# Kernel tuning notes

Hardware: AMD Instinct MI355X
Metric: run time of the kernel (lower is better)

Reference implementation:

```python
import jax, jax.numpy as jnp
import numpy as np

EPS = 1e-5  # torch F.layer_norm default

def setup_inputs() -> dict:
    key = jax.random.key(0)
    k_h, k_v = jax.random.split(key)
    B, S, d, rank = 4, 4096, 2048, 8
    h = jax.random.normal(k_h, (B, S, d), dtype=jnp.float32)
    gamma = jnp.ones((d,), dtype=jnp.float32)
    beta = jnp.zeros((d,), dtype=jnp.float32)
    V = jax.random.normal(k_v, (rank, d), dtype=jnp.float32) * 0.01
    eta = jnp.asarray(0.1, dtype=jnp.float32)
    return {"h": h, "gamma": gamma, "beta": beta, "V": V, "eta": eta}

def reference(h, gamma, beta, V, eta):
    # LayerNorm over last dim, no affine (torch F.layer_norm with only normalized_shape)
    mu = jnp.mean(h, axis=-1, keepdims=True)
    var = jnp.mean((h - mu) ** 2, axis=-1, keepdims=True)  # biased var, matches torch
    h_hat = (h - mu) * jax.lax.rsqrt(var + EPS)
    # low-rank diffusion: h_hat @ (V^T V) == (h_hat @ V^T) @ V, O(n*d*rank)
    proj = jnp.einsum('bsr,rd->bsd', jnp.einsum('bsd,rd->bsr', h_hat, V), V)
    delta_h = h_hat - proj
    e_curv = jnp.sum(delta_h ** 2, axis=-1)  # [B, S]
    eta_c = jnp.clip(eta, 0.0, 0.5)
    h_smooth = h_hat - eta_c * delta_h
    out = h_smooth * gamma + beta
    return out, e_curv
```

## Files before the change

### kernel.cpp

```cpp
#include <hip/hip_runtime.h>
#include <hip/hip_bf16.h>


constexpr int D       = 2048;
constexpr int RANK    = 8;
constexpr int BLOCK   = 256;
constexpr int ROWS_PB = 4;
constexpr float LN_EPS = 1e-5f;

using f2  = __attribute__((ext_vector_type(2))) float;
using f4v = __attribute__((ext_vector_type(4))) float;

__device__ __forceinline__ f2 f2fma(f2 a, f2 b, f2 c) {
    return __builtin_elementwise_fma(a, b, c);
}

__device__ __forceinline__ void nt_store4(float* p, float x, float y, float z, float w) {
    f4v v = {x, y, z, w};
    __builtin_nontemporal_store(v, reinterpret_cast<f4v*>(p));
}

__device__ __forceinline__ void barrier_lds() {
    asm volatile("s_waitcnt lgkmcnt(0)\n\ts_barrier" ::: "memory");
}

__device__ __forceinline__ float ordadd(float a, float b) {
    float r;
    asm volatile("v_add_f32 %0, %1, %2" : "=v"(r) : "v"(a), "v"(b));
    return r;
}

#define DPP_STAGE(v, N, MODS)                                                   \
    _Pragma("unroll")                                                           \
    for (int _n = 0; _n < N; ++_n)                                              \
        asm volatile("v_add_f32_dpp %0, %0, %0 " MODS : "+v"(v[_n]));

template<int N>
__device__ __forceinline__ void dpp_sum64_batch(float (&v)[N]) {
    static_assert(N >= 4, "need N>=4 for hazard distance");
    DPP_STAGE(v, N, "row_shr:1 row_mask:0xf bank_mask:0xf bound_ctrl:0")
    DPP_STAGE(v, N, "row_shr:2 row_mask:0xf bank_mask:0xf bound_ctrl:0")
    DPP_STAGE(v, N, "row_shr:4 row_mask:0xf bank_mask:0xf bound_ctrl:0")
    DPP_STAGE(v, N, "row_shr:8 row_mask:0xf bank_mask:0xf bound_ctrl:0")
    DPP_STAGE(v, N, "row_bcast:15 row_mask:0xa bank_mask:0xf bound_ctrl:0")
    DPP_STAGE(v, N, "row_bcast:31 row_mask:0xc bank_mask:0xf bound_ctrl:0")
}

template<int N>
__device__ __forceinline__ void qp_sum4_batch(float (&v)[N]) {
    static_assert(N >= 4, "need N>=4 for hazard distance");
    asm volatile("s_nop 1");
    DPP_STAGE(v, N, "quad_perm:[1,0,3,2] row_mask:0xf bank_mask:0xf bound_ctrl:0")
    DPP_STAGE(v, N, "quad_perm:[2,3,0,1] row_mask:0xf bank_mask:0xf bound_ctrl:0")
}

__global__ __launch_bounds__(BLOCK, 2)
void lbonorm_kernel(const float* __restrict__ h,
                    const float* __restrict__ gamma,
                    const float* __restrict__ beta,
                    const float* __restrict__ V,
                    const float* __restrict__ eta_p,
                    float* __restrict__ out,
                    float* __restrict__ e_out)
{
    const int t    = threadIdx.x;
    const int lane = t & 63;
    const int wave = t >> 6;

    const int c0 = t * 4;
    const int c1 = D / 2 + t * 4;

    __shared__ __align__(16) float red[ROWS_PB][4][12];
    __shared__ __align__(16) float ered[4][RANK];

    const size_t row0 = (size_t)blockIdx.x * ROWS_PB;

    f2 vreg[4][RANK];
    #pragma unroll
    for (int r = 0; r < RANK; ++r) {
        float4 a = *reinterpret_cast<const float4*>(V + (size_t)r * D + c0);
        float4 b = *reinterpret_cast<const float4*>(V + (size_t)r * D + c1);
        vreg[0][r] = f2{a.x, a.y}; vreg[1][r] = f2{a.z, a.w};
        vreg[2][r] = f2{b.x, b.y}; vreg[3][r] = f2{b.z, b.w};
    }
    const float4 g0 = *reinterpret_cast<const float4*>(gamma + c0);
    const float4 g1 = *reinterpret_cast<const float4*>(gamma + c1);
    const float4 bb0 = *reinterpret_cast<const float4*>(beta + c0);
    const float4 bb1 = *reinterpret_cast<const float4*>(beta + c1);
    const f2 gam[4] = {f2{g0.x,g0.y}, f2{g0.z,g0.w}, f2{g1.x,g1.y}, f2{g1.z,g1.w}};
    const f2 bet[4] = {f2{bb0.x,bb0.y}, f2{bb0.z,bb0.w}, f2{bb1.x,bb1.y}, f2{bb1.z,bb1.w}};
    const float eta = fminf(fmaxf(eta_p[0], 0.0f), 0.5f);

    float4 hx[ROWS_PB][2];
    #pragma unroll
    for (int r = 0; r < ROWS_PB; ++r) {
        hx[r][0] = *reinterpret_cast<const float4*>(h + (row0 + r) * (size_t)D + c0);
        hx[r][1] = *reinterpret_cast<const float4*>(h + (row0 + r) * (size_t)D + c1);
    }

    float vsum[RANK];
    {
        float vs[RANK];
        #pragma unroll
        for (int r = 0; r < RANK; ++r) {
            f2 v = (vreg[0][r] + vreg[1][r]) + (vreg[2][r] + vreg[3][r]);
            vs[r] = ordadd(v.x, v.y);
        }
        dpp_sum64_batch(vs);
        if (lane == 63) {
            float4* dst = reinterpret_cast<float4*>(&ered[wave][0]);
            dst[0] = make_float4(vs[0], vs[1], vs[2], vs[3]);
            dst[1] = make_float4(vs[4], vs[5], vs[6], vs[7]);
        }
        barrier_lds();
        const float4* src = reinterpret_cast<const float4*>(&ered[lane & 3][0]);
        const float4 qa = src[0], qb = src[1];
        float qv[8] = {qa.x, qa.y, qa.z, qa.w, qb.x, qb.y, qb.z, qb.w};
        qp_sum4_batch(qv);
        #pragma unroll
        for (int k = 0; k < RANK; ++k) vsum[k] = qv[k];
    }

    #pragma unroll
    for (int r = 0; r < ROWS_PB; ++r) {
        const f2 h2[4] = {f2{hx[r][0].x, hx[r][0].y}, f2{hx[r][0].z, hx[r][0].w},
                          f2{hx[r][1].x, hx[r][1].y}, f2{hx[r][1].z, hx[r][1].w}};
        float vals[10];
        {
            f2 s  = (h2[0] + h2[1]) + (h2[2] + h2[3]);
            f2 s2 = f2fma(h2[0], h2[0], f2fma(h2[1], h2[1],
                    f2fma(h2[2], h2[2], h2[3] * h2[3])));
            vals[0] = ordadd(s.x, s.y);
            vals[1] = ordadd(s2.x, s2.y);
            #pragma unroll
            for (int k = 0; k < RANK; ++k) {
                f2 d = f2fma(h2[0], vreg[0][k], f2fma(h2[1], vreg[1][k],
                       f2fma(h2[2], vreg[2][k], h2[3] * vreg[3][k])));
                vals[2 + k] = ordadd(d.x, d.y);
            }
        }
        dpp_sum64_batch(vals);

        if (lane == 63) {
            float4* dst = reinterpret_cast<float4*>(&red[r][wave][0]);
            dst[0] = make_float4(vals[0], vals[1], vals[2], vals[3]);
            dst[1] = make_float4(vals[4], vals[5], vals[6], vals[7]);
            dst[2] = make_float4(vals[8], vals[9], 0.f, 0.f);
        }
    }

    barrier_lds();

    float er[ROWS_PB];
    #pragma unroll
    for (int r = 0; r < ROWS_PB; ++r) {
        const float4* src = reinterpret_cast<const float4*>(&red[r][lane & 3][0]);
        const float4 q0 = src[0], q1 = src[1], q2 = src[2];
        float qv[10] = {q0.x, q0.y, q0.z, q0.w, q1.x, q1.y, q1.z, q1.w, q2.x, q2.y};
        qp_sum4_batch(qv);

        const float mu  = qv[0] * (1.0f / D);
        const float var = fmaxf(qv[1] * (1.0f / D) - mu * mu, 0.0f);
        const float inv = rsqrtf(var + LN_EPS);
        f2 c2[RANK];
        #pragma unroll
        for (int k = 0; k < RANK; ++k) {
            const float c = inv * (qv[2 + k] - mu * vsum[k]);
            c2[k] = f2{c, c};
        }

        const f2 h2[4] = {f2{hx[r][0].x, hx[r][0].y}, f2{hx[r][0].z, hx[r][0].w},
                          f2{hx[r][1].x, hx[r][1].y}, f2{hx[r][1].z, hx[r][1].w}};
        const f2 inv2  = f2{inv, inv};
        const f2 nmi2  = f2{-mu * inv, -mu * inv};
        const f2 neta2 = f2{-eta, -eta};
        f2 e2 = f2{0.f, 0.f};
        f2 ov[4];
        #pragma unroll
        for (int k = 0; k < 4; ++k) {
            const f2 hh = f2fma(h2[k], inv2, nmi2);
            f2 pr = c2[0] * vreg[k][0];
            #pragma unroll
            for (int q = 1; q < RANK; ++q) pr = f2fma(c2[q], vreg[k][q], pr);
            const f2 dl = hh - pr;
            e2 = f2fma(dl, dl, e2);
            const f2 sm = f2fma(neta2, dl, hh);
            ov[k] = f2fma(sm, gam[k], bet[k]);
        }

        float* orow = out + (row0 + r) * (size_t)D;
        nt_store4(orow + c0, ov[0].x, ov[0].y, ov[1].x, ov[1].y);
        nt_store4(orow + c1, ov[2].x, ov[2].y, ov[3].x, ov[3].y);

        er[r] = ordadd(e2.x, e2.y);
    }

    dpp_sum64_batch(er);
    if (lane == 63) {
        float4* dst = reinterpret_cast<float4*>(&ered[wave][0]);
        dst[0] = make_float4(er[0], er[1], er[2], er[3]);
    }
    barrier_lds();
    if (t < ROWS_PB) {
        const float e = (ered[0][t] + ered[1][t]) + (ered[2][t] + ered[3][t]);
        e_out[row0 + t] = e;
    }
}

extern "C" void kernel_launch(void* const* d_in, const int* in_sizes, int n_in,
                              void* d_out, int out_size, void* d_ws, size_t ws_size,
                              hipStream_t stream) {
    const float* h     = (const float*)d_in[0];
    const float* gamma = (const float*)d_in[1];
    const float* beta  = (const float*)d_in[2];
    const float* V     = (const float*)d_in[3];
    const float* eta   = (const float*)d_in[4];
    float* out = (float*)d_out;

    const int d = in_sizes[1];
    const long long rows = in_sizes[0] / d;
    float* e_out = out + (size_t)rows * d;

    dim3 grid((unsigned)(rows / ROWS_PB));
    lbonorm_kernel<<<grid, BLOCK, 0, stream>>>(h, gamma, beta, V, eta, out, e_out);
}
```

Before: 49.27 us.

## Process multiple row chunks per block with double-buffered register prefetch

```diff
diff --git a/kernel.cpp b/kernel.cpp
--- a/kernel.cpp
+++ b/kernel.cpp
@@ -5,7 +5,8 @@
 constexpr int D       = 2048;
 constexpr int RANK    = 8;
 constexpr int BLOCK   = 256;
-constexpr int ROWS_PB = 4;
+constexpr int ROWS_PC = 4;
+constexpr int NCHUNK  = 8;
 constexpr float LN_EPS = 1e-5f;
 
 using f2  = __attribute__((ext_vector_type(2))) float;
@@ -70,10 +71,10 @@
     const int c0 = t * 4;
     const int c1 = D / 2 + t * 4;
 
-    __shared__ __align__(16) float red[ROWS_PB][4][12];
-    __shared__ __align__(16) float ered[4][RANK];
-
-    const size_t row0 = (size_t)blockIdx.x * ROWS_PB;
+    __shared__ __align__(16) float red[2][ROWS_PC][4][12];
+    __shared__ __align__(16) float ered[4][ROWS_PC * NCHUNK];
+
+    const size_t row0 = (size_t)blockIdx.x * (ROWS_PC * NCHUNK);
 
     f2 vreg[4][RANK];
     #pragma unroll
@@ -91,11 +92,11 @@
     const f2 bet[4] = {f2{bb0.x,bb0.y}, f2{bb0.z,bb0.w}, f2{bb1.x,bb1.y}, f2{bb1.z,bb1.w}};
     const float eta = fminf(fmaxf(eta_p[0], 0.0f), 0.5f);
 
-    float4 hx[ROWS_PB][2];
+    float4 hxA[ROWS_PC][2], hxB[ROWS_PC][2];
     #pragma unroll
-    for (int r = 0; r < ROWS_PB; ++r) {
-        hx[r][0] = *reinterpret_cast<const float4*>(h + (row0 + r) * (size_t)D + c0);
-        hx[r][1] = *reinterpret_cast<const float4*>(h + (row0 + r) * (size_t)D + c1);
+    for (int r = 0; r < ROWS_PC; ++r) {
+        hxA[r][0] = *reinterpret_cast<const float4*>(h + (row0 + r) * (size_t)D + c0);
+        hxA[r][1] = *reinterpret_cast<const float4*>(h + (row0 + r) * (size_t)D + c1);
     }
 
     float vsum[RANK];
@@ -122,86 +123,101 @@
     }
 
     #pragma unroll
-    for (int r = 0; r < ROWS_PB; ++r) {
-        const f2 h2[4] = {f2{hx[r][0].x, hx[r][0].y}, f2{hx[r][0].z, hx[r][0].w},
-                          f2{hx[r][1].x, hx[r][1].y}, f2{hx[r][1].z, hx[r][1].w}};
-        float vals[10];
-        {
-            f2 s  = (h2[0] + h2[1]) + (h2[2] + h2[3]);
-            f2 s2 = f2fma(h2[0], h2[0], f2fma(h2[1], h2[1],
-                    f2fma(h2[2], h2[2], h2[3] * h2[3])));
-            vals[0] = ordadd(s.x, s.y);
-            vals[1] = ordadd(s2.x, s2.y);
+    for (int c = 0; c < NCHUNK; ++c) {
+        float4 (&cur)[ROWS_PC][2] = (c & 1) ? hxB : hxA;
+        float4 (&nxt)[ROWS_PC][2] = (c & 1) ? hxA : hxB;
+
+        if (c + 1 < NCHUNK) {
+            const size_t nrow = row0 + (size_t)(c + 1) * ROWS_PC;
+            #pragma unroll
+            for (int r = 0; r < ROWS_PC; ++r) {
+                nxt[r][0] = *reinterpret_cast<const float4*>(h + (nrow + r) * (size_t)D + c0);
+                nxt[r][1] = *reinterpret_cast<const float4*>(h + (nrow + r) * (size_t)D + c1);
+            }
+        }
+
+        #pragma unroll
+        for (int r = 0; r < ROWS_PC; ++r) {
+            const f2 h2[4] = {f2{cur[r][0].x, cur[r][0].y}, f2{cur[r][0].z, cur[r][0].w},
+                              f2{cur[r][1].x, cur[r][1].y}, f2{cur[r][1].z, cur[r][1].w}};
+            float vals[10];
+            {
+                f2 s  = (h2[0] + h2[1]) + (h2[2] + h2[3]);
+                f2 s2 = f2fma(h2[0], h2[0], f2fma(h2[1], h2[1],
+                        f2fma(h2[2], h2[2], h2[3] * h2[3])));
+                vals[0] = ordadd(s.x, s.y);
+                vals[1] = ordadd(s2.x, s2.y);
+                #pragma unroll
+                for (int k = 0; k < RANK; ++k) {
+                    f2 d = f2fma(h2[0], vreg[0][k], f2fma(h2[1], vreg[1][k],
+                           f2fma(h2[2], vreg[2][k], h2[3] * vreg[3][k])));
+                    vals[2 + k] = ordadd(d.x, d.y);
+                }
+            }
+            dpp_sum64_batch(vals);
+
+            if (lane == 63) {
+                float4* dst = reinterpret_cast<float4*>(&red[c & 1][r][wave][0]);
+                dst[0] = make_float4(vals[0], vals[1], vals[2], vals[3]);
+                dst[1] = make_float4(vals[4], vals[5], vals[6], vals[7]);
+                dst[2] = make_float4(vals[8], vals[9], 0.f, 0.f);
+            }
+        }
+
+        barrier_lds();
+
+        float er[ROWS_PC];
+        #pragma unroll
+        for (int r = 0; r < ROWS_PC; ++r) {
+            const float4* src = reinterpret_cast<const float4*>(&red[c & 1][r][lane & 3][0]);
+            const float4 q0 = src[0], q1 = src[1], q2 = src[2];
+            float qv[10] = {q0.x, q0.y, q0.z, q0.w, q1.x, q1.y, q1.z, q1.w, q2.x, q2.y};
+            qp_sum4_batch(qv);
+
+            const float mu  = qv[0] * (1.0f / D);
+            const float var = fmaxf(qv[1] * (1.0f / D) - mu * mu, 0.0f);
+            const float inv = rsqrtf(var + LN_EPS);
+            f2 c2[RANK];
             #pragma unroll
             for (int k = 0; k < RANK; ++k) {
-                f2 d = f2fma(h2[0], vreg[0][k], f2fma(h2[1], vreg[1][k],
-                       f2fma(h2[2], vreg[2][k], h2[3] * vreg[3][k])));
-                vals[2 + k] = ordadd(d.x, d.y);
-            }
-        }
-        dpp_sum64_batch(vals);
-
-        if (lane == 63) {
-            float4* dst = reinterpret_cast<float4*>(&red[r][wave][0]);
-            dst[0] = make_float4(vals[0], vals[1], vals[2], vals[3]);
-            dst[1] = make_float4(vals[4], vals[5], vals[6], vals[7]);
-            dst[2] = make_float4(vals[8], vals[9], 0.f, 0.f);
-        }
+                const float cc = inv * (qv[2 + k] - mu * vsum[k]);
+                c2[k] = f2{cc, cc};
+            }
+
+            const f2 h2[4] = {f2{cur[r][0].x, cur[r][0].y}, f2{cur[r][0].z, cur[r][0].w},
+                              f2{cur[r][1].x, cur[r][1].y}, f2{cur[r][1].z, cur[r][1].w}};
+            const f2 inv2  = f2{inv, inv};
+            const f2 nmi2  = f2{-mu * inv, -mu * inv};
+            const f2 neta2 = f2{-eta, -eta};
+            f2 e2 = f2{0.f, 0.f};
+            f2 ov[4];
+            #pragma unroll
+            for (int k = 0; k < 4; ++k) {
+                const f2 hh = f2fma(h2[k], inv2, nmi2);
+                f2 pr = c2[0] * vreg[k][0];
+                #pragma unroll
+                for (int q = 1; q < RANK; ++q) pr = f2fma(c2[q], vreg[k][q], pr);
+                const f2 dl = hh - pr;
+                e2 = f2fma(dl, dl, e2);
+                const f2 sm = f2fma(neta2, dl, hh);
+                ov[k] = f2fma(sm, gam[k], bet[k]);
+            }
+
+            float* orow = out + (row0 + (size_t)c * ROWS_PC + r) * (size_t)D;
+            nt_store4(orow + c0, ov[0].x, ov[0].y, ov[1].x, ov[1].y);
+            nt_store4(orow + c1, ov[2].x, ov[2].y, ov[3].x, ov[3].y);
+
+            er[r] = ordadd(e2.x, e2.y);
+        }
+
+        dpp_sum64_batch(er);
+        if (lane == 63)
+            *reinterpret_cast<float4*>(&ered[wave][c * ROWS_PC]) =
+                make_float4(er[0], er[1], er[2], er[3]);
     }
 
     barrier_lds();
-
-    float er[ROWS_PB];
-    #pragma unroll
-    for (int r = 0; r < ROWS_PB; ++r) {
-        const float4* src = reinterpret_cast<const float4*>(&red[r][lane & 3][0]);
-        const float4 q0 = src[0], q1 = src[1], q2 = src[2];
-        float qv[10] = {q0.x, q0.y, q0.z, q0.w, q1.x, q1.y, q1.z, q1.w, q2.x, q2.y};
-        qp_sum4_batch(qv);
-
-        const float mu  = qv[0] * (1.0f / D);
-        const float var = fmaxf(qv[1] * (1.0f / D) - mu * mu, 0.0f);
-        const float inv = rsqrtf(var + LN_EPS);
-        f2 c2[RANK];
-        #pragma unroll
-        for (int k = 0; k < RANK; ++k) {
-            const float c = inv * (qv[2 + k] - mu * vsum[k]);
-            c2[k] = f2{c, c};
-        }
-
-        const f2 h2[4] = {f2{hx[r][0].x, hx[r][0].y}, f2{hx[r][0].z, hx[r][0].w},
-                          f2{hx[r][1].x, hx[r][1].y}, f2{hx[r][1].z, hx[r][1].w}};
-        const f2 inv2  = f2{inv, inv};
-        const f2 nmi2  = f2{-mu * inv, -mu * inv};
-        const f2 neta2 = f2{-eta, -eta};
-        f2 e2 = f2{0.f, 0.f};
-        f2 ov[4];
-        #pragma unroll
-        for (int k = 0; k < 4; ++k) {
-            const f2 hh = f2fma(h2[k], inv2, nmi2);
-            f2 pr = c2[0] * vreg[k][0];
-            #pragma unroll
-            for (int q = 1; q < RANK; ++q) pr = f2fma(c2[q], vreg[k][q], pr);
-            const f2 dl = hh - pr;
-            e2 = f2fma(dl, dl, e2);
-            const f2 sm = f2fma(neta2, dl, hh);
-            ov[k] = f2fma(sm, gam[k], bet[k]);
-        }
-
-        float* orow = out + (row0 + r) * (size_t)D;
-        nt_store4(orow + c0, ov[0].x, ov[0].y, ov[1].x, ov[1].y);
-        nt_store4(orow + c1, ov[2].x, ov[2].y, ov[3].x, ov[3].y);
-
-        er[r] = ordadd(e2.x, e2.y);
-    }
-
-    dpp_sum64_batch(er);
-    if (lane == 63) {
-        float4* dst = reinterpret_cast<float4*>(&ered[wave][0]);
-        dst[0] = make_float4(er[0], er[1], er[2], er[3]);
-    }
-    barrier_lds();
-    if (t < ROWS_PB) {
+    if (t < ROWS_PC * NCHUNK) {
         const float e = (ered[0][t] + ered[1][t]) + (ered[2][t] + ered[3][t]);
         e_out[row0 + t] = e;
     }
@@ -221,6 +237,6 @@
     const long long rows = in_sizes[0] / d;
     float* e_out = out + (size_t)rows * d;
 
-    dim3 grid((unsigned)(rows / ROWS_PB));
+    dim3 grid((unsigned)(rows / (ROWS_PC * NCHUNK)));
     lbonorm_kernel<<<grid, BLOCK, 0, stream>>>(h, gamma, beta, V, eta, out, e_out);
 }
```

After: 49.11 us. About the same (-0.3%).
